# Optimization experiments

Measured on AMD Instinct MI355X. Metric: run time of the kernel, lower is better.

Reference implementation:

```python
import jax, jax.numpy as jnp
import numpy as np

N, K, D = 500_000, 256, 64  # points, prototypes, feature dim


def setup_inputs() -> dict:
    key = jax.random.key(0)
    kx, km = jax.random.split(key)
    X = jax.random.normal(kx, (N, D), dtype=jnp.float32)
    mus = jax.random.normal(km, (K, D), dtype=jnp.float32)
    return {"X": X, "mus": mus}


def reference(X, mus):
    # Faithful to vmap(lambda x: argmin(sum((mus - x)**2, axis=1)))(X),
    # but expressed with the Gram-matrix distance trick so the K*D broadcast
    # is a single GEMM instead of an O(N,K,D) elementwise intermediate.
    x_sq = jnp.sum(X * X, axis=1, keepdims=True)        # [N, 1]
    mu_sq = jnp.sum(mus * mus, axis=1)                  # [K]
    d2 = x_sq - 2.0 * (X @ mus.T) + mu_sq[None, :]      # [N, K] squared dists
    return jnp.argmin(d2, axis=1)                       # [N] int assignments
```

## Files before the change

kernel.cpp:

```cpp
#include <hip/hip_runtime.h>


#define DIM 64
#define NPROTO 256
#define NBLK 1024
#define MARGIN_ACC 0.017f

using f32x4 = __attribute__((ext_vector_type(4))) float;
using f16x8 = __attribute__((ext_vector_type(8))) _Float16;

__device__ __forceinline__ f16x8 cvt8(float4 a, float4 b) {
    f16x8 r;
    r[0] = (_Float16)a.x; r[1] = (_Float16)a.y;
    r[2] = (_Float16)a.z; r[3] = (_Float16)a.w;
    r[4] = (_Float16)b.x; r[5] = (_Float16)b.y;
    r[6] = (_Float16)b.z; r[7] = (_Float16)b.w;
    return r;
}

__global__ void __launch_bounds__(256)
argmin_mfma_kernel(const float* __restrict__ X,
                   const float* __restrict__ mus,
                   int* __restrict__ out,
                   unsigned* __restrict__ ws_count,
                   int* __restrict__ ws_list,
                   int use_list, int n) {
    __shared__ __align__(16) f16x8 s_frag[16][2][64];
    __shared__ __align__(16) float s_seed[NPROTO];

    const int tid = threadIdx.x;
    const int w = tid >> 6;
    const int l = tid & 63;
    const int lp = l & 15;
    const int lg = l >> 4;

#pragma unroll
    for (int pp = 0; pp < 4; ++pp) {
        const int p = w * 4 + pp;
        const float* src = mus + (size_t)(p * 16 + lp) * DIM + lg * 8;
        const float4 a = *(const float4*)(src);
        const float4 b = *(const float4*)(src + 4);
        const float4 c = *(const float4*)(src + 32);
        const float4 d = *(const float4*)(src + 36);
        s_frag[p][0][l] = cvt8(a, b);
        s_frag[p][1][l] = cvt8(c, d);
        float s = 0.f;
        s = fmaf(a.x, a.x, fmaf(a.y, a.y, fmaf(a.z, a.z, fmaf(a.w, a.w, s))));
        s = fmaf(b.x, b.x, fmaf(b.y, b.y, fmaf(b.z, b.z, fmaf(b.w, b.w, s))));
        s = fmaf(c.x, c.x, fmaf(c.y, c.y, fmaf(c.z, c.z, fmaf(c.w, c.w, s))));
        s = fmaf(d.x, d.x, fmaf(d.y, d.y, fmaf(d.z, d.z, fmaf(d.w, d.w, s))));
        s += __shfl_xor(s, 16);
        s += __shfl_xor(s, 32);
        if (lg == 0) s_seed[p * 16 + lp] = -0.5f * s;
    }
    __syncthreads();

    f32x4 mh[16];
#pragma unroll
    for (int p = 0; p < 16; ++p)
        mh[p] = *(const f32x4*)&s_seed[p * 16 + lg * 4];

    const int ngroups = (n + 15) / 16;
    const int NW = NBLK * 4;
    const int gwid = blockIdx.x * 4 + w;
    const int q = ngroups / NW, rr = ngroups % NW;
    const int g0 = gwid * q + (gwid < rr ? gwid : rr);
    const int cnt = q + (gwid < rr ? 1 : 0);

    const int kofs = 255 - lg * 4;

    float4 xr0, xr1, xr2, xr3;
    if (cnt > 0) {
        int row = g0 * 16 + lp; row = (row < n) ? row : (n - 1);
        const float* rp = X + (size_t)row * DIM + lg * 8;
        xr0 = *(const float4*)(rp);
        xr1 = *(const float4*)(rp + 4);
        xr2 = *(const float4*)(rp + 32);
        xr3 = *(const float4*)(rp + 36);
    }

    for (int it = 0; it < cnt; ++it) {
        const int g = g0 + it;
        const bool more = (it + 1 < cnt);

        const f16x8 bx0 = cvt8(xr0, xr1);
        const f16x8 bx1 = cvt8(xr2, xr3);

        if (more) {
            int row = (g + 1) * 16 + lp; row = (row < n) ? row : (n - 1);
            const float* rp = X + (size_t)row * DIM + lg * 8;
            xr0 = *(const float4*)(rp);
            xr1 = *(const float4*)(rp + 4);
            xr2 = *(const float4*)(rp + 32);
            xr3 = *(const float4*)(rp + 36);
        }

        float b1 = -3.4e38f, b2 = -3.4e38f;
#pragma unroll
        for (int p = 0; p < 16; ++p) {
            const f16x8 A0 = s_frag[p][0][l];
            const f16x8 A1 = s_frag[p][1][l];
            f32x4 acc = __builtin_amdgcn_mfma_f32_16x16x32_f16(
                A0, bx0, mh[p], 0, 0, 0);
            acc = __builtin_amdgcn_mfma_f32_16x16x32_f16(A1, bx1, acc,
                                                         0, 0, 0);
            float pv[4];
#pragma unroll
            for (int r = 0; r < 4; ++r) {
                unsigned u = __float_as_uint(acc[r]);
                u = (u & 0xFFFFFF00u) + (unsigned)(kofs - p * 16 - r);
                pv[r] = __uint_as_float(u);
            }
            const float t1a = fmaxf(pv[0], pv[1]), t2a = fminf(pv[0], pv[1]);
            const float t1b = fmaxf(pv[2], pv[3]), t2b = fminf(pv[2], pv[3]);
            const float p1 = fmaxf(t1a, t1b);
            const float p2 = fmaxf(fminf(t1a, t1b), fmaxf(t2a, t2b));
            const float nb2 = fmaxf(fminf(b1, p1), fmaxf(b2, p2));
            b1 = fmaxf(b1, p1);
            b2 = nb2;
        }
#pragma unroll
        for (int m = 16; m <= 32; m <<= 1) {
            const float o1 = __shfl_xor(b1, m);
            const float o2 = __shfl_xor(b2, m);
            const float nb2 = fmaxf(fminf(b1, o1), fmaxf(b2, o2));
            b1 = fmaxf(b1, o1);
            b2 = nb2;
        }

        bool fl = false;
        const int i = g * 16 + l;
        if (l < 16 && i < n) {
            const unsigned u1 = __float_as_uint(b1);
            const int k1 = 255 - (int)(u1 & 0xFFu);
            const float v1 = __uint_as_float(u1 & 0xFFFFFF00u);
            const float v2 =
                __uint_as_float(__float_as_uint(b2) & 0xFFFFFF00u);
            const bool close = (v1 - v2) < MARGIN_ACC;
            if (use_list) {
                out[i] = k1;
                fl = close;
            } else {
                out[i] = (int)((unsigned)k1 | (close ? 0x80000000u : 0u));
            }
        }
        if (use_list) {
            const unsigned long long mask = __ballot(fl);
            if (mask) {
                unsigned base = 0;
                if (l == 0)
                    base = atomicAdd(ws_count, (unsigned)__popcll(mask));
                base = __shfl(base, 0);
                if (fl)
                    ws_list[base + __popcll(mask & ((1ull << l) - 1))] = i;
            }
        }
    }
}

#define MSTRIDE 65

__global__ void __launch_bounds__(256)
fixup_lds_kernel(const float* __restrict__ X, const float* __restrict__ mus,
                 const unsigned* __restrict__ ws_count,
                 const int* __restrict__ ws_list, int* __restrict__ out) {
    __shared__ float s_mu[NPROTO * MSTRIDE];
    __shared__ float s_msq[NPROTO];

    const int tid = threadIdx.x;
    {
        const float4* mr = (const float4*)(mus + (size_t)tid * DIM);
        float q0 = 0.f, q1 = 0.f, q2 = 0.f, q3 = 0.f;
#pragma unroll
        for (int qq = 0; qq < 16; ++qq) {
            const float4 mv = mr[qq];
            const int base = tid * MSTRIDE + qq * 4;
            s_mu[base]     = mv.x;
            s_mu[base + 1] = mv.y;
            s_mu[base + 2] = mv.z;
            s_mu[base + 3] = mv.w;
            q0 = fmaf(mv.x, mv.x, q0);
            q1 = fmaf(mv.y, mv.y, q1);
            q2 = fmaf(mv.z, mv.z, q2);
            q3 = fmaf(mv.w, mv.w, q3);
        }
        s_msq[tid] = (q0 + q1) + (q2 + q3);
    }
    __syncthreads();

    const int l = tid & 63;
    const int gw = (int)((blockIdx.x * blockDim.x + tid) >> 6);
    const int NW = (int)((gridDim.x * blockDim.x) >> 6);
    const int nf = (int)*ws_count;

    for (int j = gw; j < nf; j += NW) {
        const int pt = ws_list[j];
        const float4* xr = (const float4*)(X + (size_t)pt * DIM);
        float4 xv[16];
        float a0 = 0.f, a1 = 0.f, a2 = 0.f, a3 = 0.f;
#pragma unroll
        for (int qq = 0; qq < 16; ++qq) {
            xv[qq] = xr[qq];
            a0 = fmaf(xv[qq].x, xv[qq].x, a0);
            a1 = fmaf(xv[qq].y, xv[qq].y, a1);
            a2 = fmaf(xv[qq].z, xv[qq].z, a2);
            a3 = fmaf(xv[qq].w, xv[qq].w, a3);
        }
        const float xsq = (a0 + a1) + (a2 + a3);
        float b1 = 3.4e38f;
        int k1 = 0;
#pragma unroll
        for (int e = 0; e < 4; ++e) {
            const int p = e * 64 + l;
            const float* mr = &s_mu[p * MSTRIDE];
            float d0 = 0.f, d1 = 0.f, d2 = 0.f, d3 = 0.f;
#pragma unroll
            for (int qq = 0; qq < 16; ++qq) {
                d0 = fmaf(mr[qq * 4],     xv[qq].x, d0);
                d1 = fmaf(mr[qq * 4 + 1], xv[qq].y, d1);
                d2 = fmaf(mr[qq * 4 + 2], xv[qq].z, d2);
                d3 = fmaf(mr[qq * 4 + 3], xv[qq].w, d3);
            }
            const float dot = (d0 + d1) + (d2 + d3);
            const float dd = (xsq - 2.0f * dot) + s_msq[p];
            if (dd < b1) { b1 = dd; k1 = p; }
        }
#pragma unroll
        for (int mm = 1; mm < 64; mm <<= 1) {
            const float ob = __shfl_xor(b1, mm);
            const int ok = __shfl_xor(k1, mm);
            if (ob < b1 || (ob == b1 && ok < k1)) { b1 = ob; k1 = ok; }
        }
        if (l == 0) out[pt] = k1;
    }
}

__global__ void __launch_bounds__(256)
fixup_scan_lds_kernel(const float* __restrict__ X,
                      const float* __restrict__ mus,
                      int* __restrict__ out, int n) {
    __shared__ float s_mu[NPROTO * MSTRIDE];
    __shared__ float s_msq[NPROTO];

    const int tid = threadIdx.x;
    {
        const float4* mr = (const float4*)(mus + (size_t)tid * DIM);
        float q0 = 0.f, q1 = 0.f, q2 = 0.f, q3 = 0.f;
#pragma unroll
        for (int qq = 0; qq < 16; ++qq) {
            const float4 mv = mr[qq];
            const int base = tid * MSTRIDE + qq * 4;
            s_mu[base]     = mv.x;
            s_mu[base + 1] = mv.y;
            s_mu[base + 2] = mv.z;
            s_mu[base + 3] = mv.w;
            q0 = fmaf(mv.x, mv.x, q0);
            q1 = fmaf(mv.y, mv.y, q1);
            q2 = fmaf(mv.z, mv.z, q2);
            q3 = fmaf(mv.w, mv.w, q3);
        }
        s_msq[tid] = (q0 + q1) + (q2 + q3);
    }
    __syncthreads();

    const int l = tid & 63;
    const int gw = (int)((blockIdx.x * blockDim.x + tid) >> 6);
    const int NW = (int)((gridDim.x * blockDim.x) >> 6);
    const int chunk = (n + NW - 1) / NW;
    const int base = gw * chunk;
    const int end = (base + chunk < n) ? (base + chunk) : n;

    for (int s = base; s < end; s += 64) {
        const int i = s + l;
        const int v = (i < end) ? out[i] : 0;
        const bool flg = (i < end) && ((unsigned)v & 0x80000000u);
        unsigned long long m = __ballot(flg);
        while (m) {
            const int src = (int)__ffsll((unsigned long long)m) - 1;
            m &= m - 1;
            const int pt = __shfl(i, src);
            const float4* xr = (const float4*)(X + (size_t)pt * DIM);
            float4 xv[16];
            float a0 = 0.f, a1 = 0.f, a2 = 0.f, a3 = 0.f;
#pragma unroll
            for (int qq = 0; qq < 16; ++qq) {
                xv[qq] = xr[qq];
                a0 = fmaf(xv[qq].x, xv[qq].x, a0);
                a1 = fmaf(xv[qq].y, xv[qq].y, a1);
                a2 = fmaf(xv[qq].z, xv[qq].z, a2);
                a3 = fmaf(xv[qq].w, xv[qq].w, a3);
            }
            const float xsq = (a0 + a1) + (a2 + a3);
            float b1 = 3.4e38f;
            int k1 = 0;
#pragma unroll
            for (int e = 0; e < 4; ++e) {
                const int p = e * 64 + l;
                const float* mr = &s_mu[p * MSTRIDE];
                float d0 = 0.f, d1 = 0.f, d2 = 0.f, d3 = 0.f;
#pragma unroll
                for (int qq = 0; qq < 16; ++qq) {
                    d0 = fmaf(mr[qq * 4],     xv[qq].x, d0);
                    d1 = fmaf(mr[qq * 4 + 1], xv[qq].y, d1);
                    d2 = fmaf(mr[qq * 4 + 2], xv[qq].z, d2);
                    d3 = fmaf(mr[qq * 4 + 3], xv[qq].w, d3);
                }
                const float dot = (d0 + d1) + (d2 + d3);
                const float dd = (xsq - 2.0f * dot) + s_msq[p];
                if (dd < b1) { b1 = dd; k1 = p; }
            }
#pragma unroll
            for (int mm = 1; mm < 64; mm <<= 1) {
                const float ob = __shfl_xor(b1, mm);
                const int ok = __shfl_xor(k1, mm);
                if (ob < b1 || (ob == b1 && ok < k1)) { b1 = ob; k1 = ok; }
            }
            if (l == 0) out[pt] = k1;
        }
    }
}

extern "C" void kernel_launch(void* const* d_in, const int* in_sizes, int n_in,
                              void* d_out, int out_size, void* d_ws, size_t ws_size,
                              hipStream_t stream) {
    const float* X = (const float*)d_in[0];
    const float* mus = (const float*)d_in[1];
    int* out = (int*)d_out;
    const int n = in_sizes[0] / DIM;

    unsigned* ws_count = (unsigned*)d_ws;
    int* ws_list = (int*)((char*)d_ws + 16);
    const int use_list = (ws_size >= 16 + (size_t)n * 4) ? 1 : 0;

    if (use_list) {
        hipMemsetAsync(d_ws, 0, 16, stream);
    }

    argmin_mfma_kernel<<<NBLK, 256, 0, stream>>>(X, mus, out, ws_count,
                                                 ws_list, use_list, n);
    if (use_list) {
        fixup_lds_kernel<<<512, 256, 0, stream>>>(X, mus, ws_count, ws_list,
                                                  out);
    } else {
        fixup_scan_lds_kernel<<<512, 256, 0, stream>>>(X, mus, out, n);
    }
}
```

Before: 76.57 us.

## Replace global atomic fixup list with per-wave segments and drop memset

Each wave now writes its near-tie point indices into a private fixed-size segment and records its own count, instead of using a global atomicAdd on a shared counter. This removes the atomic contention and the hipMemsetAsync launch before the main kernel. If a segment overflows, the extra points are marked in the output's high bit and rescanned by the fixup kernel. The trade-off is that the fixup kernel walks every wave's segment serially, which can load-imbalance fixup waves.

New measurement: 80.05 us. 1.05x slower.

```diff
diff --git a/kernel.cpp b/kernel.cpp
--- a/kernel.cpp
+++ b/kernel.cpp
@@ -4,6 +4,8 @@
 #define DIM 64
 #define NPROTO 256
 #define NBLK 1024
+#define NWAVE (NBLK * 4)
+#define SEGC 120
 #define MARGIN_ACC 0.017f
 
 using f32x4 = __attribute__((ext_vector_type(4))) float;
@@ -22,8 +24,8 @@
 argmin_mfma_kernel(const float* __restrict__ X,
                    const float* __restrict__ mus,
                    int* __restrict__ out,
-                   unsigned* __restrict__ ws_count,
-                   int* __restrict__ ws_list,
+                   unsigned* __restrict__ ws_cnt,
+                   int* __restrict__ ws_seg,
                    int use_list, int n) {
     __shared__ __align__(16) f16x8 s_frag[16][2][64];
     __shared__ __align__(16) float s_seed[NPROTO];
@@ -61,9 +63,8 @@
         mh[p] = *(const f32x4*)&s_seed[p * 16 + lg * 4];
 
     const int ngroups = (n + 15) / 16;
-    const int NW = NBLK * 4;
     const int gwid = blockIdx.x * 4 + w;
-    const int q = ngroups / NW, rr = ngroups % NW;
+    const int q = ngroups / NWAVE, rr = ngroups % NWAVE;
     const int g0 = gwid * q + (gwid < rr ? gwid : rr);
     const int cnt = q + (gwid < rr ? 1 : 0);
 
@@ -78,6 +79,8 @@
         xr2 = *(const float4*)(rp + 32);
         xr3 = *(const float4*)(rp + 36);
     }
+
+    unsigned fc = 0;
 
     for (int it = 0; it < cnt; ++it) {
         const int g = g0 + it;
@@ -128,42 +131,92 @@
             b2 = nb2;
         }
 
-        bool fl = false;
         const int i = g * 16 + l;
-        if (l < 16 && i < n) {
+        const bool mine = (l < 16 && i < n);
+        int k1 = 0;
+        bool close = false;
+        if (mine) {
             const unsigned u1 = __float_as_uint(b1);
-            const int k1 = 255 - (int)(u1 & 0xFFu);
+            k1 = 255 - (int)(u1 & 0xFFu);
             const float v1 = __uint_as_float(u1 & 0xFFFFFF00u);
             const float v2 =
                 __uint_as_float(__float_as_uint(b2) & 0xFFFFFF00u);
-            const bool close = (v1 - v2) < MARGIN_ACC;
-            if (use_list) {
-                out[i] = k1;
-                fl = close;
-            } else {
-                out[i] = (int)((unsigned)k1 | (close ? 0x80000000u : 0u));
+            close = (v1 - v2) < MARGIN_ACC;
+        }
+        if (use_list) {
+            const bool fl = mine && close;
+            const unsigned long long mask = __ballot(fl);
+            const unsigned off = (unsigned)__popcll(mask & ((1ull << l) - 1));
+            if (mine) {
+                const unsigned idx = fc + off;
+                if (!close) {
+                    out[i] = k1;
+                } else if (idx < SEGC) {
+                    out[i] = k1;
+                    ws_seg[gwid * SEGC + (int)idx] = i;
+                } else {
+                    out[i] = (int)((unsigned)k1 | 0x80000000u);
+                }
             }
-        }
-        if (use_list) {
-            const unsigned long long mask = __ballot(fl);
-            if (mask) {
-                unsigned base = 0;
-                if (l == 0)
-                    base = atomicAdd(ws_count, (unsigned)__popcll(mask));
-                base = __shfl(base, 0);
-                if (fl)
-                    ws_list[base + __popcll(mask & ((1ull << l) - 1))] = i;
-            }
-        }
-    }
+            fc += (unsigned)__popcll(mask);
+        } else if (mine) {
+            out[i] = (int)((unsigned)k1 | (close ? 0x80000000u : 0u));
+        }
+    }
+    if (use_list && l == 0) ws_cnt[gwid] = fc;
 }
 
 #define MSTRIDE 65
 
+__device__ __forceinline__ void fix_point(const float* __restrict__ X,
+                                          const float* s_mu,
+                                          const float* s_msq,
+                                          int* __restrict__ out,
+                                          int pt, int l) {
+    const float4* xr = (const float4*)(X + (size_t)pt * DIM);
+    float4 xv[16];
+    float a0 = 0.f, a1 = 0.f, a2 = 0.f, a3 = 0.f;
+#pragma unroll
+    for (int qq = 0; qq < 16; ++qq) {
+        xv[qq] = xr[qq];
+        a0 = fmaf(xv[qq].x, xv[qq].x, a0);
+        a1 = fmaf(xv[qq].y, xv[qq].y, a1);
+        a2 = fmaf(xv[qq].z, xv[qq].z, a2);
+        a3 = fmaf(xv[qq].w, xv[qq].w, a3);
+    }
+    const float xsq = (a0 + a1) + (a2 + a3);
+    float b1 = 3.4e38f;
+    int k1 = 0;
+#pragma unroll
+    for (int e = 0; e < 4; ++e) {
+        const int p = e * 64 + l;
+        const float* mr = &s_mu[p * MSTRIDE];
+        float d0 = 0.f, d1 = 0.f, d2 = 0.f, d3 = 0.f;
+#pragma unroll
+        for (int qq = 0; qq < 16; ++qq) {
+            d0 = fmaf(mr[qq * 4],     xv[qq].x, d0);
+            d1 = fmaf(mr[qq * 4 + 1], xv[qq].y, d1);
+            d2 = fmaf(mr[qq * 4 + 2], xv[qq].z, d2);
+            d3 = fmaf(mr[qq * 4 + 3], xv[qq].w, d3);
+        }
+        const float dot = (d0 + d1) + (d2 + d3);
+        const float dd = (xsq - 2.0f * dot) + s_msq[p];
+        if (dd < b1) { b1 = dd; k1 = p; }
+    }
+#pragma unroll
+    for (int mm = 1; mm < 64; mm <<= 1) {
+        const float ob = __shfl_xor(b1, mm);
+        const int ok = __shfl_xor(k1, mm);
+        if (ob < b1 || (ob == b1 && ok < k1)) { b1 = ob; k1 = ok; }
+    }
+    if (l == 0) out[pt] = k1;
+}
+
 __global__ void __launch_bounds__(256)
-fixup_lds_kernel(const float* __restrict__ X, const float* __restrict__ mus,
-                 const unsigned* __restrict__ ws_count,
-                 const int* __restrict__ ws_list, int* __restrict__ out) {
+fixup_seg_kernel(const float* __restrict__ X, const float* __restrict__ mus,
+                 const unsigned* __restrict__ ws_cnt,
+                 const int* __restrict__ ws_seg,
+                 int* __restrict__ out, int n) {
     __shared__ float s_mu[NPROTO * MSTRIDE];
     __shared__ float s_msq[NPROTO];
 
@@ -189,49 +242,37 @@
     __syncthreads();
 
     const int l = tid & 63;
-    const int gw = (int)((blockIdx.x * blockDim.x + tid) >> 6);
-    const int NW = (int)((gridDim.x * blockDim.x) >> 6);
-    const int nf = (int)*ws_count;
-
-    for (int j = gw; j < nf; j += NW) {
-        const int pt = ws_list[j];
-        const float4* xr = (const float4*)(X + (size_t)pt * DIM);
-        float4 xv[16];
-        float a0 = 0.f, a1 = 0.f, a2 = 0.f, a3 = 0.f;
-#pragma unroll
-        for (int qq = 0; qq < 16; ++qq) {
-            xv[qq] = xr[qq];
-            a0 = fmaf(xv[qq].x, xv[qq].x, a0);
-            a1 = fmaf(xv[qq].y, xv[qq].y, a1);
-            a2 = fmaf(xv[qq].z, xv[qq].z, a2);
-            a3 = fmaf(xv[qq].w, xv[qq].w, a3);
-        }
-        const float xsq = (a0 + a1) + (a2 + a3);
-        float b1 = 3.4e38f;
-        int k1 = 0;
-#pragma unroll
-        for (int e = 0; e < 4; ++e) {
-            const int p = e * 64 + l;
-            const float* mr = &s_mu[p * MSTRIDE];
-            float d0 = 0.f, d1 = 0.f, d2 = 0.f, d3 = 0.f;
-#pragma unroll
-            for (int qq = 0; qq < 16; ++qq) {
-                d0 = fmaf(mr[qq * 4],     xv[qq].x, d0);
-                d1 = fmaf(mr[qq * 4 + 1], xv[qq].y, d1);
-                d2 = fmaf(mr[qq * 4 + 2], xv[qq].z, d2);
-                d3 = fmaf(mr[qq * 4 + 3], xv[qq].w, d3);
+    const int fw = (int)((blockIdx.x * blockDim.x + tid) >> 6);
+    const int NWf = (int)((gridDim.x * blockDim.x) >> 6);
+
+    const int ngroups = (n + 15) / 16;
+    const int q = ngroups / NWAVE, rr = ngroups % NWAVE;
+
+    for (int wid = fw; wid < NWAVE; wid += NWf) {
+        const unsigned c = ws_cnt[wid];
+        const unsigned m = (c < SEGC) ? c : SEGC;
+        for (unsigned j = 0; j < m; ++j) {
+            const int pt = ws_seg[wid * SEGC + (int)j];
+            fix_point(X, s_mu, s_msq, out, pt, l);
+        }
+        if (c > SEGC) {
+            const int g0 = wid * q + (wid < rr ? wid : rr);
+            const int gc = q + (wid < rr ? 1 : 0);
+            const int beg = g0 * 16;
+            int end = (g0 + gc) * 16;
+            end = (end < n) ? end : n;
+            for (int s = beg + l; s - l < end; s += 64) {
+                const bool flg =
+                    (s < end) && ((unsigned)out[s] & 0x80000000u);
+                unsigned long long mk = __ballot(flg);
+                while (mk) {
+                    const int src = (int)__ffsll((unsigned long long)mk) - 1;
+                    mk &= mk - 1;
+                    const int pt = __shfl(s, src);
+                    fix_point(X, s_mu, s_msq, out, pt, l);
+                }
             }
-            const float dot = (d0 + d1) + (d2 + d3);
-            const float dd = (xsq - 2.0f * dot) + s_msq[p];
-            if (dd < b1) { b1 = dd; k1 = p; }
-        }
-#pragma unroll
-        for (int mm = 1; mm < 64; mm <<= 1) {
-            const float ob = __shfl_xor(b1, mm);
-            const int ok = __shfl_xor(k1, mm);
-            if (ob < b1 || (ob == b1 && ok < k1)) { b1 = ob; k1 = ok; }
-        }
-        if (l == 0) out[pt] = k1;
+        }
     }
 }
 
@@ -279,43 +320,7 @@
             const int src = (int)__ffsll((unsigned long long)m) - 1;
             m &= m - 1;
             const int pt = __shfl(i, src);
-            const float4* xr = (const float4*)(X + (size_t)pt * DIM);
-            float4 xv[16];
-            float a0 = 0.f, a1 = 0.f, a2 = 0.f, a3 = 0.f;
-#pragma unroll
-            for (int qq = 0; qq < 16; ++qq) {
-                xv[qq] = xr[qq];
-                a0 = fmaf(xv[qq].x, xv[qq].x, a0);
-                a1 = fmaf(xv[qq].y, xv[qq].y, a1);
-                a2 = fmaf(xv[qq].z, xv[qq].z, a2);
-                a3 = fmaf(xv[qq].w, xv[qq].w, a3);
-            }
-            const float xsq = (a0 + a1) + (a2 + a3);
-            float b1 = 3.4e38f;
-            int k1 = 0;
-#pragma unroll
-            for (int e = 0; e < 4; ++e) {
-                const int p = e * 64 + l;
-                const float* mr = &s_mu[p * MSTRIDE];
-                float d0 = 0.f, d1 = 0.f, d2 = 0.f, d3 = 0.f;
-#pragma unroll
-                for (int qq = 0; qq < 16; ++qq) {
-                    d0 = fmaf(mr[qq * 4],     xv[qq].x, d0);
-                    d1 = fmaf(mr[qq * 4 + 1], xv[qq].y, d1);
-                    d2 = fmaf(mr[qq * 4 + 2], xv[qq].z, d2);
-                    d3 = fmaf(mr[qq * 4 + 3], xv[qq].w, d3);
-                }
-                const float dot = (d0 + d1) + (d2 + d3);
-                const float dd = (xsq - 2.0f * dot) + s_msq[p];
-                if (dd < b1) { b1 = dd; k1 = p; }
-            }
-#pragma unroll
-            for (int mm = 1; mm < 64; mm <<= 1) {
-                const float ob = __shfl_xor(b1, mm);
-                const int ok = __shfl_xor(k1, mm);
-                if (ob < b1 || (ob == b1 && ok < k1)) { b1 = ob; k1 = ok; }
-            }
-            if (l == 0) out[pt] = k1;
+            fix_point(X, s_mu, s_msq, out, pt, l);
         }
     }
 }
@@ -328,19 +333,16 @@
     int* out = (int*)d_out;
     const int n = in_sizes[0] / DIM;
 
-    unsigned* ws_count = (unsigned*)d_ws;
-    int* ws_list = (int*)((char*)d_ws + 16);
-    const int use_list = (ws_size >= 16 + (size_t)n * 4) ? 1 : 0;
-
+    unsigned* ws_cnt = (unsigned*)d_ws;
+    int* ws_seg = (int*)((char*)d_ws + NWAVE * 4);
+    const size_t need = (size_t)NWAVE * 4 + (size_t)NWAVE * SEGC * 4;
+    const int use_list = (ws_size >= need) ? 1 : 0;
+
+    argmin_mfma_kernel<<<NBLK, 256, 0, stream>>>(X, mus, out, ws_cnt,
+                                                 ws_seg, use_list, n);
     if (use_list) {
-        hipMemsetAsync(d_ws, 0, 16, stream);
-    }
-
-    argmin_mfma_kernel<<<NBLK, 256, 0, stream>>>(X, mus, out, ws_count,
-                                                 ws_list, use_list, n);
-    if (use_list) {
-        fixup_lds_kernel<<<512, 256, 0, stream>>>(X, mus, ws_count, ws_list,
-                                                  out);
+        fixup_seg_kernel<<<512, 256, 0, stream>>>(X, mus, ws_cnt, ws_seg,
+                                                  out, n);
     } else {
         fixup_scan_lds_kernel<<<512, 256, 0, stream>>>(X, mus, out, n);
     }
```
